# Kernel optimization log

Hardware: AMD Instinct MI355X
Metric: run time of the kernel (lower is better)

The kernel has to match this reference:

```python
import jax, jax.numpy as jnp
import numpy as np

N = 160000          # active voxels / points
C = 128             # embed_channels
K = 27              # 3x3x3 submanifold conv kernel volume
NUM_CLUSTERS = 2048
BN_EPS = 1e-5


def setup_inputs() -> dict:
    key = jax.random.key(0)
    ks = jax.random.split(key, 16)
    s = 0.05
    inp = {
        "feat": jax.random.normal(ks[0], (N, C), jnp.float32),
        "cluster0": jax.random.randint(ks[1], (N,), 0, NUM_CLUSTERS, jnp.int32),
        "cluster1": jax.random.randint(ks[2], (N,), 0, NUM_CLUSTERS, jnp.int32),
        "cluster2": jax.random.randint(ks[3], (N,), 0, NUM_CLUSTERS, jnp.int32),
        "nbr_idx": jax.random.randint(ks[4], (N, K), 0, N, jnp.int32),
        "nbr_mask": jax.random.randint(ks[5], (N, K), 0, 2, jnp.int32) > 0,
        "lw_W": jax.random.normal(ks[6], (3, C, C), jnp.float32) * s,
        "lw_gamma": jnp.ones((3, C), jnp.float32),
        "lw_beta": jnp.zeros((3, C), jnp.float32),
        "w_W": jax.random.normal(ks[7], (3, C, C), jnp.float32) * s,
        "proj_W": jax.random.normal(ks[8], (4, C, C), jnp.float32) * s,
        "proj_gamma": jnp.ones((4, C), jnp.float32),
        "proj_beta": jnp.zeros((4, C), jnp.float32),
        "adaptive_W": jax.random.normal(ks[9], (C, 3), jnp.float32) * s,
        "fuse_W": jax.random.normal(ks[10], (2 * C, C), jnp.float32) * s,
        "fuse_gamma": jnp.ones((C,), jnp.float32),
        "fuse_beta": jnp.zeros((C,), jnp.float32),
        "conv_W": jax.random.normal(ks[11], (2, K, C, C), jnp.float32) * 0.02,
        "conv_gamma": jnp.ones((2, C), jnp.float32),
        "conv_beta": jnp.zeros((2, C), jnp.float32),
    }
    return inp


def _bn(x, gamma, beta):
    # BatchNorm1d, training mode: per-channel stats over points, biased var
    m = jnp.mean(x, axis=0)
    v = jnp.var(x, axis=0)
    return (x - m) * jax.lax.rsqrt(v + BN_EPS) * gamma + beta


def _seg_sum(x, seg):
    return jax.ops.segment_sum(x, seg, num_segments=NUM_CLUSTERS)


def _seg_mean(x, seg):
    s = _seg_sum(x, seg)
    cnt = jax.ops.segment_sum(jnp.ones((x.shape[0], 1), x.dtype), seg,
                              num_segments=NUM_CLUSTERS)
    return s / jnp.maximum(cnt, 1.0)


def _subm_conv(x, W, nbr_idx, nbr_mask):
    # submanifold 3x3x3 conv on active sites: masked gather + per-offset GEMM
    m = nbr_mask.astype(x.dtype)  # [N, K]
    out = jnp.zeros_like(x)
    for k in range(K):
        out = out + (x[nbr_idx[:, k]] * m[:, k:k + 1]) @ W[k]
    return out


def reference(feat, cluster0, cluster1, cluster2, nbr_idx, nbr_mask,
              lw_W, lw_gamma, lw_beta, w_W, proj_W, proj_gamma, proj_beta,
              adaptive_W, fuse_W, fuse_gamma, fuse_beta,
              conv_W, conv_gamma, conv_beta):
    clusters = [cluster0, cluster1, cluster2]
    feats = []
    for i, cl in enumerate(clusters):
        pw = jax.nn.relu(_bn(feat @ lw_W[i], lw_gamma[i], lw_beta[i]))
        pw = pw - _seg_mean(pw, cl)[cl]
        pw = pw @ w_W[i]
        pw = jnp.exp(pw - jnp.max(pw))                      # global max
        pw = pw / (_seg_sum(pw, cl)[cl] + 1e-6)
        pfeat = jax.nn.relu(_bn(feat @ proj_W[i], proj_gamma[i], proj_beta[i])) * pw
        pfeat = _seg_sum(pfeat, cl)[cl]
        feats.append(pfeat)

    adp = jax.nn.softmax(feat @ adaptive_W, axis=1)          # [N, 3]
    feats = jnp.stack(feats, axis=1)                         # [N, 3, C]
    fused_branch = jnp.einsum('ln,lnc->lc', adp, feats)

    f = jax.nn.relu(_bn(feat @ proj_W[3], proj_gamma[3], proj_beta[3]))
    f = jnp.concatenate([f, fused_branch], axis=1)           # [N, 2C]
    f = jax.nn.relu(_bn(f @ fuse_W, fuse_gamma, fuse_beta)) + feat

    res = f
    h = _subm_conv(f, conv_W[0], nbr_idx, nbr_mask)
    h = jax.nn.relu(_bn(h, conv_gamma[0], conv_beta[0]))
    h = _subm_conv(h, conv_W[1], nbr_idx, nbr_mask)
    h = _bn(h, conv_gamma[1], conv_beta[1])
    return jax.nn.relu(h + res)
```

## Files before the change

kernel.cpp:

```cpp
#include <hip/hip_runtime.h>
#include <stdint.h>

#define N_PTS 160000
#define C 128
#define K27 27
#define NCLU 2048
#define BN_EPS 1e-5f
#define KP 136
#define KP2 264

typedef float f32x4 __attribute__((ext_vector_type(4)));
typedef short s16x8 __attribute__((ext_vector_type(8)));

__device__ __forceinline__ float bf2f(unsigned short u){
  union { unsigned int i; float f; } v; v.i = ((unsigned int)u) << 16; return v.f;
}
__device__ __forceinline__ unsigned short f2bf(float f){
  union { float f; unsigned int i; } v; v.f = f;
  unsigned int u = v.i;
  u += 0x7FFFu + ((u >> 16) & 1u);
  return (unsigned short)(u >> 16);
}
__device__ __forceinline__ unsigned int pk(float a, float b){
  return (unsigned int)f2bf(a) | ((unsigned int)f2bf(b) << 16);
}
__device__ __forceinline__ void up2(int w, float& a, float& b){
  a = bf2f((unsigned short)(w & 0xFFFF));
  b = bf2f((unsigned short)(((unsigned int)w) >> 16));
}
__device__ __forceinline__ unsigned int encf(float f){
  union { float f; unsigned int i; } v; v.f = f;
  return ((int)v.i < 0) ? ~v.i : (v.i | 0x80000000u);
}
__device__ __forceinline__ float decf(unsigned int e){
  union { unsigned int i; float f; } v;
  v.i = ((int)e < 0) ? (e ^ 0x80000000u) : ~e;
  return v.f;
}
__device__ __forceinline__ void bn_coef(const float* st, const float* gamma, const float* beta,
                                        int c, float& sc, float& sh){
  float mean = st[c] * (1.0f / N_PTS);
  float var  = st[C + c] * (1.0f / N_PTS) - mean * mean;
  float g = gamma[c] * rsqrtf(fmaxf(var, 0.f) + BN_EPS);
  sc = g; sh = beta[c] - mean * g;
}

__global__ void k_prep_weights(const float* __restrict__ lw, const float* __restrict__ w,
                               const float* __restrict__ proj, const float* __restrict__ conv,
                               const float* __restrict__ fuse,
                               unsigned short* __restrict__ tlw, unsigned short* __restrict__ tw,
                               unsigned short* __restrict__ tproj, unsigned short* __restrict__ tconv,
                               unsigned short* __restrict__ tfuse)
{
  int z = blockIdx.x, tid = threadIdx.x;
  if (z < 64){
    const float* src; unsigned short* dst; bool swz = false;
    if (z < 3){ src = lw + z*16384; dst = tlw + z*16384; }
    else if (z < 6){ src = w + (z-3)*16384; dst = tw + (z-3)*16384; }
    else if (z < 10){ src = proj + (z-6)*16384; dst = tproj + (z-6)*16384; }
    else { src = conv + (z-10)*16384; dst = tconv + (z-10)*16384; swz = true; }
    for (int i = tid; i < 16384; i += 256){
      int n = i >> 7, k = i & 127;
      int pos = swz ? (n*128 + (((k >> 3) ^ (n & 7)) << 3) + (k & 7)) : i;
      dst[pos] = f2bf(src[k*128 + n]);
    }
  } else {
    for (int i = tid; i < 32768; i += 256){
      int n = i >> 8, k = i & 255;
      tfuse[i] = f2bf(fuse[k*128 + n]);
    }
  }
}

__global__ void k_detect_mask(const unsigned int* __restrict__ mw, int* __restrict__ mmode)
{
  __shared__ int flag;
  if (threadIdx.x == 0) flag = 0;
  __syncthreads();
  for (int i = threadIdx.x; i < 4096; i += 256)
    if (mw[i] > 1u) flag = 1;
  __syncthreads();
  if (threadIdx.x == 0) *mmode = flag;
}

__global__ void k_hist(const int* __restrict__ c0, const int* __restrict__ c1,
                       const int* __restrict__ c2, int* __restrict__ hist)
{
  int idx = blockIdx.x*blockDim.x + threadIdx.x;
  int stride = gridDim.x*blockDim.x;
  for (; idx < 3*N_PTS; idx += stride){
    int j = idx / N_PTS, r = idx - j*N_PTS;
    const int* cp = (j==0)?c0:((j==1)?c1:c2);
    atomicAdd(&hist[j*NCLU + cp[r]], 1);
  }
}

__global__ void k_prefix(const int* __restrict__ hist, int* __restrict__ starts,
                         int* __restrict__ cursor)
{
  int j = blockIdx.x, tid = threadIdx.x;
  __shared__ int buf[NCLU];
  __shared__ int csum[256];
  for (int i = tid; i < NCLU; i += 256) buf[i] = hist[j*NCLU + i];
  __syncthreads();
  int s = 0;
  #pragma unroll
  for (int k = 0; k < 8; k++) s += buf[tid*8 + k];
  csum[tid] = s;
  __syncthreads();
  if (tid == 0){
    int run = 0;
    for (int i = 0; i < 256; i++){ int t = csum[i]; csum[i] = run; run += t; }
  }
  __syncthreads();
  int acc = csum[tid];
  #pragma unroll
  for (int k = 0; k < 8; k++){
    int i = tid*8 + k;
    starts[j*(NCLU+1) + i] = acc;
    cursor[j*NCLU + i] = acc;
    acc += buf[i];
  }
  if (tid == 255) starts[j*(NCLU+1) + NCLU] = acc;
}

__global__ void k_scatter(const int* __restrict__ c0, const int* __restrict__ c1,
                          const int* __restrict__ c2, int* __restrict__ cursor,
                          int* __restrict__ perm)
{
  int idx = blockIdx.x*blockDim.x + threadIdx.x;
  int stride = gridDim.x*blockDim.x;
  for (; idx < 3*N_PTS; idx += stride){
    int j = idx / N_PTS, r = idx - j*N_PTS;
    const int* cp = (j==0)?c0:((j==1)?c1:c2);
    int cl = cp[r];
    int slot = atomicAdd(&cursor[j*NCLU + cl], 1);
    perm[j*N_PTS + slot] = r;
  }
}

template<int V>
__global__ void k_seg(const unsigned short* __restrict__ X, const unsigned short* __restrict__ X2,
                      const int* __restrict__ perm, const int* __restrict__ starts,
                      const float* __restrict__ st, const float* __restrict__ gamma,
                      const float* __restrict__ beta, const unsigned int* __restrict__ genc,
                      const float* __restrict__ S2, float* __restrict__ S)
{
  __shared__ float red[16*128];
  const int cl = blockIdx.x;
  const int p0 = starts[cl], p1 = starts[cl+1];
  const int g = threadIdx.x >> 4, s = threadIdx.x & 15;
  const int c0 = s * 8;
  float sc[8], sh[8], den[8];
  if (V == 0 || V == 2){
    #pragma unroll
    for (int j = 0; j < 8; j++) bn_coef(st, gamma, beta, c0 + j, sc[j], sh[j]);
  }
  float gm = 0.f;
  if (V >= 1) gm = decf(*genc);
  if (V == 2){
    #pragma unroll
    for (int j = 0; j < 8; j++) den[j] = S2[cl*C + c0 + j] + 1e-6f;
  }
  float acc[8];
  #pragma unroll
  for (int j = 0; j < 8; j++) acc[j] = 0.f;
  for (int p = p0 + g; p < p1; p += 16){
    int row = perm[p];
    int4 v = *(const int4*)(X + (size_t)row*C + c0);
    float f[8];
    up2(v.x, f[0], f[1]); up2(v.y, f[2], f[3]); up2(v.z, f[4], f[5]); up2(v.w, f[6], f[7]);
    if (V == 0){
      #pragma unroll
      for (int j = 0; j < 8; j++) acc[j] += fmaxf(f[j]*sc[j] + sh[j], 0.f);
    } else if (V == 1){
      #pragma unroll
      for (int j = 0; j < 8; j++) acc[j] += __expf(f[j] - gm);
    } else {
      int4 v2 = *(const int4*)(X2 + (size_t)row*C + c0);
      float x2[8];
      up2(v2.x, x2[0], x2[1]); up2(v2.y, x2[2], x2[3]); up2(v2.z, x2[4], x2[5]); up2(v2.w, x2[6], x2[7]);
      #pragma unroll
      for (int j = 0; j < 8; j++)
        acc[j] += fmaxf(f[j]*sc[j] + sh[j], 0.f) * __expf(x2[j] - gm) / den[j];
    }
  }
  #pragma unroll
  for (int j = 0; j < 8; j++) red[g*128 + c0 + j] = acc[j];
  __syncthreads();
  if (threadIdx.x < 128){
    float t = 0.f;
    #pragma unroll
    for (int gg = 0; gg < 16; gg++) t += red[gg*128 + threadIdx.x];
    S[cl*C + threadIdx.x] = t;
  }
}

__global__ void k_adp(const float* __restrict__ feat, const float* __restrict__ aW,
                      float* __restrict__ adp, unsigned short* __restrict__ featb)
{
  __shared__ float wsh[384];
  int tid = threadIdx.x;
  for (int i = tid; i < 384; i += 256) wsh[i] = aW[i];
  __syncthreads();
  int gidx = blockIdx.x*256 + tid;
  int stride = gridDim.x*256;
  for (int t4 = gidx; t4 < N_PTS*4; t4 += stride){
    int row = t4 >> 2, part = t4 & 3;
    float e0=0.f, e1=0.f, e2=0.f;
    const float* fr = feat + (size_t)row*C + part*32;
    unsigned int pb[16];
    #pragma unroll
    for (int c = 0; c < 32; c += 4){
      float4 v = *(const float4*)(fr + c);
      int cc = part*32 + c;
      e0 += v.x*wsh[cc*3+0] + v.y*wsh[(cc+1)*3+0] + v.z*wsh[(cc+2)*3+0] + v.w*wsh[(cc+3)*3+0];
      e1 += v.x*wsh[cc*3+1] + v.y*wsh[(cc+1)*3+1] + v.z*wsh[(cc+2)*3+1] + v.w*wsh[(cc+3)*3+1];
      e2 += v.x*wsh[cc*3+2] + v.y*wsh[(cc+1)*3+2] + v.z*wsh[(cc+2)*3+2] + v.w*wsh[(cc+3)*3+2];
      pb[(c>>1)]   = pk(v.x, v.y);
      pb[(c>>1)+1] = pk(v.z, v.w);
    }
    if (featb){
      int4* dst = (int4*)(featb + (size_t)row*C + part*32);
      dst[0] = make_int4(pb[0], pb[1], pb[2], pb[3]);
      dst[1] = make_int4(pb[4], pb[5], pb[6], pb[7]);
      dst[2] = make_int4(pb[8], pb[9], pb[10], pb[11]);
      dst[3] = make_int4(pb[12], pb[13], pb[14], pb[15]);
    }
    e0 += __shfl_xor(e0, 1); e0 += __shfl_xor(e0, 2);
    e1 += __shfl_xor(e1, 1); e1 += __shfl_xor(e1, 2);
    e2 += __shfl_xor(e2, 1); e2 += __shfl_xor(e2, 2);
    if (part == 0){
      float m = fmaxf(e0, fmaxf(e1, e2));
      float p0 = __expf(e0-m), p1 = __expf(e1-m), p2 = __expf(e2-m);
      float inv = 1.f/(p0+p1+p2);
      adp[row*3+0] = p0*inv; adp[row*3+1] = p1*inv; adp[row*3+2] = p2*inv;
    }
  }
}

__device__ __forceinline__ void gemm_stats_epi(float* csum, float* csq, float* sred,
                                               int wave, int l4, int l16, int tid,
                                               float* __restrict__ stats)
{
  #pragma unroll
  for (int t = 0; t < 8; t++){
    csum[t] += __shfl_xor(csum[t], 16); csum[t] += __shfl_xor(csum[t], 32);
    csq[t]  += __shfl_xor(csq[t], 16);  csq[t]  += __shfl_xor(csq[t], 32);
  }
  if (l4 == 0){
    #pragma unroll
    for (int t = 0; t < 8; t++){
      sred[wave*128 + t*16 + l16] = csum[t];
      sred[512 + wave*128 + t*16 + l16] = csq[t];
    }
  }
  __syncthreads();
  if (tid < 128){
    float s = 0.f, q = 0.f;
    #pragma unroll
    for (int w2 = 0; w2 < 4; w2++){ s += sred[w2*128 + tid]; q += sred[512 + w2*128 + tid]; }
    atomicAdd(&stats[tid], s);
    atomicAdd(&stats[C + tid], q);
  }
}

template<typename AT>
__device__ __forceinline__ void stage_A(const AT* __restrict__ A, unsigned short* As,
                                        int row0, int r, int s)
{
  #pragma unroll
  for (int p = 0; p < 4; p++){
    int rr = r + p * 16;
    if constexpr (sizeof(AT) == 2){
      *(int4*)(As + rr * KP + s * 8) =
        *(const int4*)((const unsigned short*)A + (size_t)(row0 + rr) * C + s * 8);
    } else {
      const float4* ap = (const float4*)((const float*)A + (size_t)(row0 + rr) * C + s * 8);
      float4 x = ap[0], y = ap[1];
      *(int4*)(As + rr * KP + s * 8) =
        make_int4(pk(x.x,x.y), pk(x.z,x.w), pk(y.x,y.y), pk(y.z,y.w));
    }
  }
}

template<typename AT>
__global__ __launch_bounds__(256, 3)
void k_gemm_plain(const AT* __restrict__ A, const unsigned short* __restrict__ Bt,
                  unsigned short* __restrict__ Out, float* __restrict__ stats)
{
  __shared__ unsigned short As[64 * KP];
  __shared__ unsigned short Bs[128 * KP];
  const int tid = threadIdx.x;
  const int row0 = blockIdx.x * 64;
  const int r = tid >> 4, s = tid & 15;
  stage_A<AT>(A, As, row0, r, s);
  #pragma unroll
  for (int p = 0; p < 8; p++){
    int nn = r + p * 16;
    *(int4*)(Bs + nn * KP + s * 8) = *(const int4*)(Bt + nn * C + s * 8);
  }
  __syncthreads();
  const int lane = tid & 63, wave = tid >> 6;
  const int l16 = lane & 15, l4 = lane >> 4, m0 = wave * 16;
  f32x4 acc[8];
  #pragma unroll
  for (int t = 0; t < 8; t++) acc[t] = (f32x4){0.f,0.f,0.f,0.f};
  #pragma unroll
  for (int kk = 0; kk < 4; kk++){
    s16x8 a = *(const s16x8*)(As + (m0 + l16) * KP + kk * 32 + l4 * 8);
    #pragma unroll
    for (int t = 0; t < 8; t++){
      s16x8 b = *(const s16x8*)(Bs + (t * 16 + l16) * KP + kk * 32 + l4 * 8);
      acc[t] = __builtin_amdgcn_mfma_f32_16x16x32_bf16(a, b, acc[t], 0, 0, 0);
    }
  }
  float csum[8], csq[8];
  #pragma unroll
  for (int t = 0; t < 8; t++){
    float ss = 0.f, qq = 0.f;
    #pragma unroll
    for (int q = 0; q < 4; q++){
      float v = acc[t][q];
      int grow = row0 + m0 + l4 * 4 + q;
      Out[(size_t)grow * C + t * 16 + l16] = f2bf(v);
      ss += v; qq += v*v;
    }
    csum[t] = ss; csq[t] = qq;
  }
  __syncthreads();
  gemm_stats_epi(csum, csq, (float*)As, wave, l4, l16, tid, stats);
}

template<typename AT>
__global__ __launch_bounds__(256, 3)
void k_gemm_dual(const AT* __restrict__ A,
                 const unsigned short* __restrict__ Bt0, const unsigned short* __restrict__ Bt1,
                 unsigned short* __restrict__ Out0, unsigned short* __restrict__ Out1,
                 float* __restrict__ stats0, float* __restrict__ stats1)
{
  __shared__ unsigned short As[64 * KP];
  __shared__ unsigned short Bs[128 * KP];
  const int tid = threadIdx.x;
  const int row0 = blockIdx.x * 64;
  const int r = tid >> 4, s = tid & 15;
  const int lane = tid & 63, wave = tid >> 6;
  const int l16 = lane & 15, l4 = lane >> 4, m0 = wave * 16;

  stage_A<AT>(A, As, row0, r, s);
  #pragma unroll
  for (int p = 0; p < 8; p++){
    int nn = r + p * 16;
    *(int4*)(Bs + nn * KP + s * 8) = *(const int4*)(Bt0 + nn * C + s * 8);
  }
  __syncthreads();

  f32x4 acc[8];
  float csum0[8], csq0[8], csum1[8], csq1[8];

  #pragma unroll
  for (int t = 0; t < 8; t++) acc[t] = (f32x4){0.f,0.f,0.f,0.f};
  #pragma unroll
  for (int kk = 0; kk < 4; kk++){
    s16x8 a = *(const s16x8*)(As + (m0 + l16) * KP + kk * 32 + l4 * 8);
    #pragma unroll
    for (int t = 0; t < 8; t++){
      s16x8 b = *(const s16x8*)(Bs + (t * 16 + l16) * KP + kk * 32 + l4 * 8);
      acc[t] = __builtin_amdgcn_mfma_f32_16x16x32_bf16(a, b, acc[t], 0, 0, 0);
    }
  }
  #pragma unroll
  for (int t = 0; t < 8; t++){
    float ss = 0.f, qq = 0.f;
    #pragma unroll
    for (int q = 0; q < 4; q++){
      float v = acc[t][q];
      int grow = row0 + m0 + l4 * 4 + q;
      Out0[(size_t)grow * C + t * 16 + l16] = f2bf(v);
      ss += v; qq += v*v;
    }
    csum0[t] = ss; csq0[t] = qq;
  }
  __syncthreads();
  #pragma unroll
  for (int p = 0; p < 8; p++){
    int nn = r + p * 16;
    *(int4*)(Bs + nn * KP + s * 8) = *(const int4*)(Bt1 + nn * C + s * 8);
  }
  __syncthreads();

  #pragma unroll
  for (int t = 0; t < 8; t++) acc[t] = (f32x4){0.f,0.f,0.f,0.f};
  #pragma unroll
  for (int kk = 0; kk < 4; kk++){
    s16x8 a = *(const s16x8*)(As + (m0 + l16) * KP + kk * 32 + l4 * 8);
    #pragma unroll
    for (int t = 0; t < 8; t++){
      s16x8 b = *(const s16x8*)(Bs + (t * 16 + l16) * KP + kk * 32 + l4 * 8);
      acc[t] = __builtin_amdgcn_mfma_f32_16x16x32_bf16(a, b, acc[t], 0, 0, 0);
    }
  }
  #pragma unroll
  for (int t = 0; t < 8; t++){
    float ss = 0.f, qq = 0.f;
    #pragma unroll
    for (int q = 0; q < 4; q++){
      float v = acc[t][q];
      int grow = row0 + m0 + l4 * 4 + q;
      Out1[(size_t)grow * C + t * 16 + l16] = f2bf(v);
      ss += v; qq += v*v;
    }
    csum1[t] = ss; csq1[t] = qq;
  }
  __syncthreads();
  gemm_stats_epi(csum0, csq0, (float*)As, wave, l4, l16, tid, stats0);
  __syncthreads();
  gemm_stats_epi(csum1, csq1, (float*)As, wave, l4, l16, tid, stats1);
}

__global__ __launch_bounds__(256, 3)
void k_gemm_center(const unsigned short* __restrict__ PW, const unsigned short* __restrict__ Bt,
                   const int* __restrict__ cla, const float* __restrict__ S1,
                   const int* __restrict__ cnt, const float* __restrict__ st,
                   const float* __restrict__ gamma, const float* __restrict__ beta,
                   unsigned short* __restrict__ Out, unsigned int* __restrict__ gmax)
{
  __shared__ unsigned short As[64 * KP];
  __shared__ unsigned short Bs[128 * KP];
  __shared__ float wred[4];
  const int tid = threadIdx.x;
  const int row0 = blockIdx.x * 64;
  const int r = tid >> 4, s = tid & 15;
  float sc[8], sh[8];
  #pragma unroll
  for (int j = 0; j < 8; j++) bn_coef(st, gamma, beta, s*8 + j, sc[j], sh[j]);
  #pragma unroll
  for (int p = 0; p < 4; p++){
    int rr = r + p * 16;
    int grow = row0 + rr;
    int cl = cla[grow];
    float inv = 1.f / fmaxf(1.f, (float)cnt[cl]);
    int4 v = *(const int4*)(PW + (size_t)grow * C + s * 8);
    const float4* mp = (const float4*)(S1 + cl * C + s * 8);
    float4 ma = mp[0], mb = mp[1];
    float f[8];
    up2(v.x, f[0], f[1]); up2(v.y, f[2], f[3]); up2(v.z, f[4], f[5]); up2(v.w, f[6], f[7]);
    float m8[8] = {ma.x,ma.y,ma.z,ma.w,mb.x,mb.y,mb.z,mb.w};
    float o[8];
    #pragma unroll
    for (int j = 0; j < 8; j++) o[j] = fmaxf(f[j]*sc[j] + sh[j], 0.f) - m8[j]*inv;
    *(int4*)(As + rr * KP + s * 8) = make_int4(pk(o[0],o[1]), pk(o[2],o[3]), pk(o[4],o[5]), pk(o[6],o[7]));
  }
  #pragma unroll
  for (int p = 0; p < 8; p++){
    int nn = r + p * 16;
    *(int4*)(Bs + nn * KP + s * 8) = *(const int4*)(Bt + nn * C + s * 8);
  }
  __syncthreads();
  const int lane = tid & 63, wave = tid >> 6;
  const int l16 = lane & 15, l4 = lane >> 4, m0 = wave * 16;
  f32x4 acc[8];
  #pragma unroll
  for (int t = 0; t < 8; t++) acc[t] = (f32x4){0.f,0.f,0.f,0.f};
  #pragma unroll
  for (int kk = 0; kk < 4; kk++){
    s16x8 a = *(const s16x8*)(As + (m0 + l16) * KP + kk * 32 + l4 * 8);
    #pragma unroll
    for (int t = 0; t < 8; t++){
      s16x8 b = *(const s16x8*)(Bs + (t * 16 + l16) * KP + kk * 32 + l4 * 8);
      acc[t] = __builtin_amdgcn_mfma_f32_16x16x32_bf16(a, b, acc[t], 0, 0, 0);
    }
  }
  float mx = -3.4e38f;
  #pragma unroll
  for (int t = 0; t < 8; t++){
    #pragma unroll
    for (int q = 0; q < 4; q++){
      int grow = row0 + m0 + l4 * 4 + q;
      unsigned short ob = f2bf(acc[t][q]);
      Out[(size_t)grow * C + t * 16 + l16] = ob;
      mx = fmaxf(mx, bf2f(ob));
    }
  }
  #pragma unroll
  for (int off = 32; off; off >>= 1) mx = fmaxf(mx, __shfl_xor(mx, off));
  if ((tid & 63) == 0) wred[tid >> 6] = mx;
  __syncthreads();
  if (tid == 0){
    float m = fmaxf(fmaxf(wred[0], wred[1]), fmaxf(wred[2], wred[3]));
    atomicMax(gmax, encf(m));
  }
}

__global__ __launch_bounds__(256, 2)
void k_gemm_fuse(const unsigned short* __restrict__ XP3, const float* __restrict__ adp,
                 const int* __restrict__ cl0, const int* __restrict__ cl1,
                 const int* __restrict__ cl2, const float* __restrict__ S3,
                 const float* __restrict__ st, const float* __restrict__ gamma,
                 const float* __restrict__ beta, const unsigned short* __restrict__ Bt,
                 unsigned short* __restrict__ Out, float* __restrict__ stats)
{
  __shared__ unsigned short As[64 * KP2];
  __shared__ unsigned short Bs[128 * KP];
  __shared__ float scs[C], shs[C];
  const int tid = threadIdx.x;
  if (tid < C){ float a, b; bn_coef(st, gamma, beta, tid, a, b); scs[tid] = a; shs[tid] = b; }
  __syncthreads();
  const int row0 = blockIdx.x * 64;
  const int r8 = tid >> 5, s = tid & 31;
  const int r = tid >> 4, s16i = tid & 15;
  #pragma unroll
  for (int p = 0; p < 8; p++){
    int rr = r8 + p * 8;
    int grow = row0 + rr;
    if (s < 16){
      int c0 = s * 8;
      int4 v = *(const int4*)(XP3 + (size_t)grow * C + c0);
      float f0,f1,f2,f3,f4,f5,f6,f7;
      up2(v.x,f0,f1); up2(v.y,f2,f3); up2(v.z,f4,f5); up2(v.w,f6,f7);
      float o0 = fmaxf(f0*scs[c0+0]+shs[c0+0],0.f), o1 = fmaxf(f1*scs[c0+1]+shs[c0+1],0.f);
      float o2 = fmaxf(f2*scs[c0+2]+shs[c0+2],0.f), o3 = fmaxf(f3*scs[c0+3]+shs[c0+3],0.f);
      float o4 = fmaxf(f4*scs[c0+4]+shs[c0+4],0.f), o5 = fmaxf(f5*scs[c0+5]+shs[c0+5],0.f);
      float o6 = fmaxf(f6*scs[c0+6]+shs[c0+6],0.f), o7 = fmaxf(f7*scs[c0+7]+shs[c0+7],0.f);
      *(int4*)(As + rr * KP2 + c0) = make_int4(pk(o0,o1), pk(o2,o3), pk(o4,o5), pk(o6,o7));
    } else {
      int c0 = (s - 16) * 8;
      float a0 = adp[grow*3+0], a1 = adp[grow*3+1], a2 = adp[grow*3+2];
      const float* p0 = S3 + (size_t)cl0[grow] * C + c0;
      const float* p1 = S3 + (size_t)NCLU * C + (size_t)cl1[grow] * C + c0;
      const float* p2 = S3 + (size_t)2 * NCLU * C + (size_t)cl2[grow] * C + c0;
      float o[8];
      #pragma unroll
      for (int j = 0; j < 8; j++) o[j] = a0*p0[j] + a1*p1[j] + a2*p2[j];
      *(int4*)(As + rr * KP2 + 128 + c0) = make_int4(pk(o[0],o[1]), pk(o[2],o[3]), pk(o[4],o[5]), pk(o[6],o[7]));
    }
  }
  const int lane = tid & 63, wave = tid >> 6;
  const int l16 = lane & 15, l4 = lane >> 4, m0 = wave * 16;
  f32x4 acc[8];
  #pragma unroll
  for (int t = 0; t < 8; t++) acc[t] = (f32x4){0.f,0.f,0.f,0.f};
  #pragma unroll
  for (int h = 0; h < 2; h++){
    if (h) __syncthreads();
    #pragma unroll
    for (int p = 0; p < 8; p++){
      int nn = r + p * 16;
      *(int4*)(Bs + nn * KP + s16i * 8) = *(const int4*)(Bt + nn * 256 + h * 128 + s16i * 8);
    }
    __syncthreads();
    #pragma unroll
    for (int kk = 0; kk < 4; kk++){
      s16x8 a = *(const s16x8*)(As + (m0 + l16) * KP2 + h * 128 + kk * 32 + l4 * 8);
      #pragma unroll
      for (int t = 0; t < 8; t++){
        s16x8 b = *(const s16x8*)(Bs + (t * 16 + l16) * KP + kk * 32 + l4 * 8);
        acc[t] = __builtin_amdgcn_mfma_f32_16x16x32_bf16(a, b, acc[t], 0, 0, 0);
      }
    }
  }
  float csum[8], csq[8];
  #pragma unroll
  for (int t = 0; t < 8; t++){
    float ss = 0.f, qq = 0.f;
    #pragma unroll
    for (int q = 0; q < 4; q++){
      float v = acc[t][q];
      int grow = row0 + m0 + l4 * 4 + q;
      Out[(size_t)grow * C + t * 16 + l16] = f2bf(v);
      ss += v; qq += v*v;
    }
    csum[t] = ss; csq[t] = qq;
  }
  __syncthreads();
  gemm_stats_epi(csum, csq, (float*)As, wave, l4, l16, tid, stats);
}

__device__ __forceinline__ int ld_midx(const int* __restrict__ nbr, const void* __restrict__ maskp,
                                       int mm, int g){
  bool on = mm ? (((const unsigned char*)maskp)[g] != 0)
               : (((const int*)maskp)[g] != 0);
  int v = nbr[g];
  return on ? v : -1;
}

template<typename OT>
__global__ __launch_bounds__(512, 2)
void k_conv(const unsigned short* __restrict__ In, const unsigned short* __restrict__ Wt,
            const int* __restrict__ nbr, const void* __restrict__ maskp,
            const int* __restrict__ mmode, OT* __restrict__ Out, float* __restrict__ stats)
{
  __shared__ unsigned short Bs[2][128*128];
  const int tid = threadIdx.x;
  const int lane = tid & 63, wave = tid >> 6;
  const int l16 = lane & 15, l4 = lane >> 4;
  const int row0 = blockIdx.x * 256;
  const int mm = *mmode;
  const int r0g = row0 + wave*32 + l16;
  const int r1g = r0g + 16;
  const s16x8 z8 = (s16x8){0,0,0,0,0,0,0,0};

  auto stage_B = [&](int buf, int k){
    const char* gsrc = (const char*)(Wt + k*16384);
    char* lbase = (char*)&Bs[buf][0];
    #pragma unroll
    for (int p = 0; p < 4; p++){
      int chunk = p*512 + wave*64;
      __builtin_amdgcn_global_load_lds(
        (const unsigned int*)(gsrc + (size_t)(chunk + lane)*16),
        (unsigned int*)(lbase + (size_t)chunk*16), 16, 0, 0);
    }
  };

  f32x4 acc0[8], acc1[8];
  #pragma unroll
  for (int t = 0; t < 8; t++){ acc0[t] = (f32x4){0.f,0.f,0.f,0.f}; acc1[t] = (f32x4){0.f,0.f,0.f,0.f}; }

  s16x8 A0[8], A1[8];
  auto gather = [&](s16x8* dA, int gi0, int gi1){
    #pragma unroll
    for (int kk = 0; kk < 4; kk++){
      dA[kk]   = (gi0 >= 0) ? *(const s16x8*)(In + (size_t)gi0*C + kk*32 + l4*8) : z8;
      dA[kk+4] = (gi1 >= 0) ? *(const s16x8*)(In + (size_t)gi1*C + kk*32 + l4*8) : z8;
    }
  };
  auto compute = [&](const s16x8* a, int buf){
    #pragma unroll
    for (int kk = 0; kk < 4; kk++){
      #pragma unroll
      for (int t = 0; t < 8; t++){
        int n = t*16 + l16;
        s16x8 b = *(const s16x8*)(&Bs[buf][n*128 + ((((kk<<2)|l4) ^ (n & 7)) << 3)]);
        acc0[t] = __builtin_amdgcn_mfma_f32_16x16x32_bf16(a[kk],   b, acc0[t], 0, 0, 0);
        acc1[t] = __builtin_amdgcn_mfma_f32_16x16x32_bf16(a[kk+4], b, acc1[t], 0, 0, 0);
      }
    }
  };

  stage_B(0, 0);
  int i0 = ld_midx(nbr, maskp, mm, r0g*K27 + 0);
  int i1 = ld_midx(nbr, maskp, mm, r1g*K27 + 0);
  gather(A0, i0, i1);
  i0 = ld_midx(nbr, maskp, mm, r0g*K27 + 1);
  i1 = ld_midx(nbr, maskp, mm, r1g*K27 + 1);
  __syncthreads();

  #pragma unroll 1
  for (int kb = 0; kb < 13; kb++){
    const int k = kb * 2;
    stage_B(1, k + 1);
    gather(A1, i0, i1);
    i0 = ld_midx(nbr, maskp, mm, r0g*K27 + k + 2);
    i1 = ld_midx(nbr, maskp, mm, r1g*K27 + k + 2);
    compute(A0, 0);
    __syncthreads();
    stage_B(0, k + 2);
    gather(A0, i0, i1);
    if (kb < 12){
      i0 = ld_midx(nbr, maskp, mm, r0g*K27 + k + 3);
      i1 = ld_midx(nbr, maskp, mm, r1g*K27 + k + 3);
    }
    compute(A1, 1);
    __syncthreads();
  }
  compute(A0, 0);

  float csum[8], csq[8];
  #pragma unroll
  for (int t = 0; t < 8; t++){
    float ss = 0.f, qq = 0.f;
    #pragma unroll
    for (int q = 0; q < 4; q++){
      float v = acc0[t][q];
      int grow = row0 + wave*32 + l4*4 + q;
      if constexpr (sizeof(OT) == 2) Out[(size_t)grow * C + t*16 + l16] = f2bf(v);
      else                           Out[(size_t)grow * C + t*16 + l16] = v;
      ss += v; qq += v*v;
    }
    #pragma unroll
    for (int q = 0; q < 4; q++){
      float v = acc1[t][q];
      int grow = row0 + wave*32 + 16 + l4*4 + q;
      if constexpr (sizeof(OT) == 2) Out[(size_t)grow * C + t*16 + l16] = f2bf(v);
      else                           Out[(size_t)grow * C + t*16 + l16] = v;
      ss += v; qq += v*v;
    }
    csum[t] = ss; csq[t] = qq;
  }
  #pragma unroll
  for (int t = 0; t < 8; t++){
    csum[t] += __shfl_xor(csum[t], 16); csum[t] += __shfl_xor(csum[t], 32);
    csq[t]  += __shfl_xor(csq[t], 16);  csq[t]  += __shfl_xor(csq[t], 32);
  }
  __syncthreads();
  float* sred = (float*)Bs;
  if (l4 == 0){
    #pragma unroll
    for (int t = 0; t < 8; t++){
      sred[wave*128 + t*16 + l16] = csum[t];
      sred[1024 + wave*128 + t*16 + l16] = csq[t];
    }
  }
  __syncthreads();
  if (tid < 128){
    float s = 0.f, q = 0.f;
    #pragma unroll
    for (int w2 = 0; w2 < 8; w2++){ s += sred[w2*128 + tid]; q += sred[1024 + w2*128 + tid]; }
    atomicAdd(&stats[tid], s);
    atomicAdd(&stats[C + tid], q);
  }
}

template<int RELU>
__global__ void k_bnapply(const unsigned short* __restrict__ X, unsigned short* __restrict__ Y,
                          const float* __restrict__ st, const float* __restrict__ gamma,
                          const float* __restrict__ beta)
{
  const int total = N_PTS * 16;
  for (int idx = blockIdx.x*blockDim.x + threadIdx.x; idx < total; idx += gridDim.x*blockDim.x){
    int c0 = (idx & 15) * 8;
    int4 v = *(const int4*)(X + (size_t)idx * 8);
    float f[8];
    up2(v.x, f[0], f[1]); up2(v.y, f[2], f[3]); up2(v.z, f[4], f[5]); up2(v.w, f[6], f[7]);
    float o[8];
    #pragma unroll
    for (int j = 0; j < 8; j++){
      float sc, sh; bn_coef(st, gamma, beta, c0 + j, sc, sh);
      float t = f[j] * sc + sh;
      if (RELU) t = fmaxf(t, 0.f);
      o[j] = t;
    }
    *(int4*)(Y + (size_t)idx * 8) = make_int4(pk(o[0],o[1]), pk(o[2],o[3]), pk(o[4],o[5]), pk(o[6],o[7]));
  }
}

__global__ void k_fres(const unsigned short* __restrict__ G, const float* __restrict__ st,
                       const float* __restrict__ gamma, const float* __restrict__ beta,
                       const float* __restrict__ feat, unsigned short* __restrict__ FB)
{
  const int total = N_PTS * 16;
  for (int idx = blockIdx.x*blockDim.x + threadIdx.x; idx < total; idx += gridDim.x*blockDim.x){
    int c0 = (idx & 15) * 8;
    int4 v = *(const int4*)(G + (size_t)idx * 8);
    float f[8];
    up2(v.x, f[0], f[1]); up2(v.y, f[2], f[3]); up2(v.z, f[4], f[5]); up2(v.w, f[6], f[7]);
    const float4* fp = (const float4*)(feat + (size_t)idx * 8);
    float4 fa = fp[0], fb4 = fp[1];
    float fe[8] = {fa.x,fa.y,fa.z,fa.w,fb4.x,fb4.y,fb4.z,fb4.w};
    float o[8];
    #pragma unroll
    for (int j = 0; j < 8; j++){
      float sc, sh; bn_coef(st, gamma, beta, c0 + j, sc, sh);
      o[j] = fmaxf(f[j]*sc + sh, 0.f) + fe[j];
    }
    *(int4*)(FB + (size_t)idx * 8) = make_int4(pk(o[0],o[1]), pk(o[2],o[3]), pk(o[4],o[5]), pk(o[6],o[7]));
  }
}

__global__ void k_final(float* __restrict__ H2, const float* __restrict__ st,
                        const float* __restrict__ gamma, const float* __restrict__ beta,
                        const unsigned short* __restrict__ FB)
{
  const int total = N_PTS * 16;
  for (int idx = blockIdx.x*blockDim.x + threadIdx.x; idx < total; idx += gridDim.x*blockDim.x){
    int c0 = (idx & 15) * 8;
    float4* hp = (float4*)(H2 + (size_t)idx * 8);
    float4 a = hp[0], b = hp[1];
    int4 vf = *(const int4*)(FB + (size_t)idx * 8);
    float fr[8];
    up2(vf.x, fr[0], fr[1]); up2(vf.y, fr[2], fr[3]); up2(vf.z, fr[4], fr[5]); up2(vf.w, fr[6], fr[7]);
    float h[8] = {a.x,a.y,a.z,a.w,b.x,b.y,b.z,b.w};
    #pragma unroll
    for (int j = 0; j < 8; j++){
      float sc, sh; bn_coef(st, gamma, beta, c0 + j, sc, sh);
      h[j] = fmaxf(h[j]*sc + sh + fr[j], 0.f);
    }
    hp[0] = make_float4(h[0],h[1],h[2],h[3]);
    hp[1] = make_float4(h[4],h[5],h[6],h[7]);
  }
}

extern "C" void kernel_launch(void* const* d_in, const int* in_sizes, int n_in,
                              void* d_out, int out_size, void* d_ws, size_t ws_size,
                              hipStream_t stream)
{
  (void)in_sizes; (void)n_in; (void)out_size;
  const float* feat   = (const float*)d_in[0];
  const int* cls[3]   = {(const int*)d_in[1], (const int*)d_in[2], (const int*)d_in[3]};
  const int* nbr      = (const int*)d_in[4];
  const void* mask    = d_in[5];
  const float* lw_W   = (const float*)d_in[6];
  const float* lw_g   = (const float*)d_in[7];
  const float* lw_b   = (const float*)d_in[8];
  const float* w_W    = (const float*)d_in[9];
  const float* proj_W = (const float*)d_in[10];
  const float* proj_g = (const float*)d_in[11];
  const float* proj_b = (const float*)d_in[12];
  const float* adW    = (const float*)d_in[13];
  const float* fuse_W = (const float*)d_in[14];
  const float* fuse_g = (const float*)d_in[15];
  const float* fuse_b = (const float*)d_in[16];
  const float* conv_W = (const float*)d_in[17];
  const float* conv_g = (const float*)d_in[18];
  const float* conv_b = (const float*)d_in[19];

  char* w = (char*)d_ws;
  float*          stats  = (float*)(w + 0);
  unsigned int*   gmax   = (unsigned int*)(w + 10240);
  int*            mmode  = (int*)(w + 10240 + 16);
  int*            hist   = (int*)(w + 10496);
  int*            starts = (int*)(w + 35072);
  int*            cursor = (int*)(w + 59904);
  int*            perm   = (int*)(w + 84480);
  float*          S1     = (float*)(w + 2004480);
  float*          S2     = (float*)(w + 3053056);
  float*          S3     = (float*)(w + 4101632);
  float*          adp    = (float*)(w + 7247360);
  unsigned short* tlw    = (unsigned short*)(w + 9167360);
  unsigned short* tw     = (unsigned short*)(w + 9265664);
  unsigned short* tproj  = (unsigned short*)(w + 9363968);
  unsigned short* tfuse  = (unsigned short*)(w + 9495040);
  unsigned short* tconv  = (unsigned short*)(w + 9560576);
  unsigned short* B1     = (unsigned short*)(w + 11330048);
  unsigned short* B2     = (unsigned short*)(w + 52290048);
  unsigned short* B3     = (unsigned short*)(w + 93250048);
  const bool useb = ws_size >= (size_t)175170048;
  unsigned short* featb = useb ? (unsigned short*)(w + 134210048) : nullptr;

  hipMemsetAsync(d_ws, 0, 35072, stream);

  k_prep_weights<<<65, 256, 0, stream>>>(lw_W, w_W, proj_W, conv_W, fuse_W,
                                         tlw, tw, tproj, tconv, tfuse);
  k_detect_mask<<<1, 256, 0, stream>>>((const unsigned int*)mask, mmode);
  k_hist<<<1024, 256, 0, stream>>>(cls[0], cls[1], cls[2], hist);
  k_prefix<<<3, 256, 0, stream>>>(hist, starts, cursor);
  k_scatter<<<1024, 256, 0, stream>>>(cls[0], cls[1], cls[2], cursor, perm);
  k_adp<<<2500, 256, 0, stream>>>(feat, adW, adp, featb);

  if (useb) k_gemm_plain<unsigned short><<<2500, 256, 0, stream>>>(featb, tlw, B1, stats);
  else      k_gemm_plain<float><<<2500, 256, 0, stream>>>(feat, tlw, B1, stats);

  for (int i = 0; i < 3; i++){
    k_seg<0><<<2048, 256, 0, stream>>>(B1, nullptr, perm + i*N_PTS, starts + i*(NCLU+1),
                                       stats + i*256, lw_g + i*C, lw_b + i*C, nullptr, nullptr, S1);
    k_gemm_center<<<2500, 256, 0, stream>>>(B1, tw + i*16384, cls[i], S1, hist + i*NCLU,
                                            stats + i*256, lw_g + i*C, lw_b + i*C, B3, gmax + i);
    k_seg<1><<<2048, 256, 0, stream>>>(B3, nullptr, perm + i*N_PTS, starts + i*(NCLU+1),
                                       nullptr, nullptr, nullptr, gmax + i, nullptr, S2);
    const unsigned short* w0 = tproj + i*16384;
    const unsigned short* w1 = (i < 2) ? (tlw + (i+1)*16384) : (tproj + 3*16384);
    float* st1 = (i < 2) ? (stats + (i+1)*256) : (stats + 6*256);
    if (useb) k_gemm_dual<unsigned short><<<2500, 256, 0, stream>>>(featb, w0, w1, B2, B1,
                                                                    stats + (3+i)*256, st1);
    else      k_gemm_dual<float><<<2500, 256, 0, stream>>>(feat, w0, w1, B2, B1,
                                                           stats + (3+i)*256, st1);
    k_seg<2><<<2048, 256, 0, stream>>>(B2, B3, perm + i*N_PTS, starts + i*(NCLU+1),
                                       stats + (3+i)*256, proj_g + i*C, proj_b + i*C,
                                       gmax + i, S2, S3 + (size_t)i*NCLU*C);
  }

  k_gemm_fuse<<<2500, 256, 0, stream>>>(B1, adp, cls[0], cls[1], cls[2], S3,
                                        stats + 6*256, proj_g + 3*C, proj_b + 3*C, tfuse,
                                        B2, stats + 7*256);
  k_fres<<<2048, 256, 0, stream>>>(B2, stats + 7*256, fuse_g, fuse_b, feat, B3);

  k_conv<unsigned short><<<625, 512, 0, stream>>>(B3, tconv, nbr, mask, mmode, B1, stats + 8*256);
  k_bnapply<1><<<2048, 256, 0, stream>>>(B1, B2, stats + 8*256, conv_g, conv_b);
  k_conv<float><<<625, 512, 0, stream>>>(B2, tconv + 27*16384, nbr, mask, mmode,
                                         (float*)d_out, stats + 9*256);
  k_final<<<2048, 256, 0, stream>>>((float*)d_out, stats + 9*256, conv_g + C, conv_b + C, B3);
}
```

Baseline: 1.380 ms.

## Fuse softmax-denominator and weighted segment sums; halve conv rows per block

The separate exp-sum segment kernel is merged into a new per-cluster kernel. It first computes the softmax denominator in shared memory, then does the weighted pooled sum in a second pass over the same cluster rows. This removes one launch per branch and the S2 global round trip, at the cost of reading X2 twice within the block. Separately, the submanifold conv now handles 128 rows per block instead of 256, with one accumulator set and a launch-bounds hint of 4 blocks. This trades fewer registers and more blocks for twice as many weight stagings into LDS overall.

```diff
diff --git a/kernel.cpp b/kernel.cpp
--- a/kernel.cpp
+++ b/kernel.cpp
@@ -140,28 +140,19 @@
 }
 
 template<int V>
-__global__ void k_seg(const unsigned short* __restrict__ X, const unsigned short* __restrict__ X2,
+__global__ void k_seg(const unsigned short* __restrict__ X,
                       const int* __restrict__ perm, const int* __restrict__ starts,
                       const float* __restrict__ st, const float* __restrict__ gamma,
-                      const float* __restrict__ beta, const unsigned int* __restrict__ genc,
-                      const float* __restrict__ S2, float* __restrict__ S)
+                      const float* __restrict__ beta, float* __restrict__ S)
 {
   __shared__ float red[16*128];
   const int cl = blockIdx.x;
   const int p0 = starts[cl], p1 = starts[cl+1];
   const int g = threadIdx.x >> 4, s = threadIdx.x & 15;
   const int c0 = s * 8;
-  float sc[8], sh[8], den[8];
-  if (V == 0 || V == 2){
-    #pragma unroll
-    for (int j = 0; j < 8; j++) bn_coef(st, gamma, beta, c0 + j, sc[j], sh[j]);
-  }
-  float gm = 0.f;
-  if (V >= 1) gm = decf(*genc);
-  if (V == 2){
-    #pragma unroll
-    for (int j = 0; j < 8; j++) den[j] = S2[cl*C + c0 + j] + 1e-6f;
-  }
+  float sc[8], sh[8];
+  #pragma unroll
+  for (int j = 0; j < 8; j++) bn_coef(st, gamma, beta, c0 + j, sc[j], sh[j]);
   float acc[8];
   #pragma unroll
   for (int j = 0; j < 8; j++) acc[j] = 0.f;
@@ -170,20 +161,8 @@
     int4 v = *(const int4*)(X + (size_t)row*C + c0);
     float f[8];
     up2(v.x, f[0], f[1]); up2(v.y, f[2], f[3]); up2(v.z, f[4], f[5]); up2(v.w, f[6], f[7]);
-    if (V == 0){
-      #pragma unroll
-      for (int j = 0; j < 8; j++) acc[j] += fmaxf(f[j]*sc[j] + sh[j], 0.f);
-    } else if (V == 1){
-      #pragma unroll
-      for (int j = 0; j < 8; j++) acc[j] += __expf(f[j] - gm);
-    } else {
-      int4 v2 = *(const int4*)(X2 + (size_t)row*C + c0);
-      float x2[8];
-      up2(v2.x, x2[0], x2[1]); up2(v2.y, x2[2], x2[3]); up2(v2.z, x2[4], x2[5]); up2(v2.w, x2[6], x2[7]);
-      #pragma unroll
-      for (int j = 0; j < 8; j++)
-        acc[j] += fmaxf(f[j]*sc[j] + sh[j], 0.f) * __expf(x2[j] - gm) / den[j];
-    }
+    #pragma unroll
+    for (int j = 0; j < 8; j++) acc[j] += fmaxf(f[j]*sc[j] + sh[j], 0.f);
   }
   #pragma unroll
   for (int j = 0; j < 8; j++) red[g*128 + c0 + j] = acc[j];
@@ -193,6 +172,72 @@
     #pragma unroll
     for (int gg = 0; gg < 16; gg++) t += red[gg*128 + threadIdx.x];
     S[cl*C + threadIdx.x] = t;
+  }
+}
+
+__global__ void k_seg12(const unsigned short* __restrict__ XP, const unsigned short* __restrict__ X2,
+                        const int* __restrict__ perm, const int* __restrict__ starts,
+                        const float* __restrict__ st, const float* __restrict__ gamma,
+                        const float* __restrict__ beta, const unsigned int* __restrict__ genc,
+                        float* __restrict__ S3)
+{
+  __shared__ float red[16*128];
+  const int cl = blockIdx.x;
+  const int p0 = starts[cl], p1 = starts[cl+1];
+  const int g = threadIdx.x >> 4, s = threadIdx.x & 15;
+  const int c0 = s * 8;
+  const float gm = decf(*genc);
+  float sc[8], sh[8];
+  #pragma unroll
+  for (int j = 0; j < 8; j++) bn_coef(st, gamma, beta, c0 + j, sc[j], sh[j]);
+
+  float acc[8];
+  #pragma unroll
+  for (int j = 0; j < 8; j++) acc[j] = 0.f;
+  for (int p = p0 + g; p < p1; p += 16){
+    int row = perm[p];
+    int4 v2 = *(const int4*)(X2 + (size_t)row*C + c0);
+    float x2[8];
+    up2(v2.x, x2[0], x2[1]); up2(v2.y, x2[2], x2[3]); up2(v2.z, x2[4], x2[5]); up2(v2.w, x2[6], x2[7]);
+    #pragma unroll
+    for (int j = 0; j < 8; j++) acc[j] += __expf(x2[j] - gm);
+  }
+  #pragma unroll
+  for (int j = 0; j < 8; j++) red[g*128 + c0 + j] = acc[j];
+  __syncthreads();
+  if (threadIdx.x < 128){
+    float t = 0.f;
+    #pragma unroll
+    for (int gg = 0; gg < 16; gg++) t += red[gg*128 + threadIdx.x];
+    red[threadIdx.x] = t;
+  }
+  __syncthreads();
+  float den[8];
+  #pragma unroll
+  for (int j = 0; j < 8; j++) den[j] = red[c0 + j] + 1e-6f;
+  __syncthreads();
+
+  #pragma unroll
+  for (int j = 0; j < 8; j++) acc[j] = 0.f;
+  for (int p = p0 + g; p < p1; p += 16){
+    int row = perm[p];
+    int4 v  = *(const int4*)(XP + (size_t)row*C + c0);
+    int4 v2 = *(const int4*)(X2 + (size_t)row*C + c0);
+    float f[8], x2[8];
+    up2(v.x, f[0], f[1]); up2(v.y, f[2], f[3]); up2(v.z, f[4], f[5]); up2(v.w, f[6], f[7]);
+    up2(v2.x, x2[0], x2[1]); up2(v2.y, x2[2], x2[3]); up2(v2.z, x2[4], x2[5]); up2(v2.w, x2[6], x2[7]);
+    #pragma unroll
+    for (int j = 0; j < 8; j++)
+      acc[j] += fmaxf(f[j]*sc[j] + sh[j], 0.f) * __expf(x2[j] - gm) / den[j];
+  }
+  #pragma unroll
+  for (int j = 0; j < 8; j++) red[g*128 + c0 + j] = acc[j];
+  __syncthreads();
+  if (threadIdx.x < 128){
+    float t = 0.f;
+    #pragma unroll
+    for (int gg = 0; gg < 16; gg++) t += red[gg*128 + threadIdx.x];
+    S3[cl*C + threadIdx.x] = t;
   }
 }
 
@@ -585,7 +630,7 @@
 }
 
 template<typename OT>
-__global__ __launch_bounds__(512, 2)
+__global__ __launch_bounds__(512, 4)
 void k_conv(const unsigned short* __restrict__ In, const unsigned short* __restrict__ Wt,
             const int* __restrict__ nbr, const void* __restrict__ maskp,
             const int* __restrict__ mmode, OT* __restrict__ Out, float* __restrict__ stats)
@@ -594,10 +639,9 @@
   const int tid = threadIdx.x;
   const int lane = tid & 63, wave = tid >> 6;
   const int l16 = lane & 15, l4 = lane >> 4;
-  const int row0 = blockIdx.x * 256;
+  const int row0 = blockIdx.x * 128;
   const int mm = *mmode;
-  const int r0g = row0 + wave*32 + l16;
-  const int r1g = r0g + 16;
+  const int rg = row0 + wave*16 + l16;
   const s16x8 z8 = (s16x8){0,0,0,0,0,0,0,0};
 
   auto stage_B = [&](int buf, int k){
@@ -612,17 +656,15 @@
     }
   };
 
-  f32x4 acc0[8], acc1[8];
-  #pragma unroll
-  for (int t = 0; t < 8; t++){ acc0[t] = (f32x4){0.f,0.f,0.f,0.f}; acc1[t] = (f32x4){0.f,0.f,0.f,0.f}; }
-
-  s16x8 A0[8], A1[8];
-  auto gather = [&](s16x8* dA, int gi0, int gi1){
-    #pragma unroll
-    for (int kk = 0; kk < 4; kk++){
-      dA[kk]   = (gi0 >= 0) ? *(const s16x8*)(In + (size_t)gi0*C + kk*32 + l4*8) : z8;
-      dA[kk+4] = (gi1 >= 0) ? *(const s16x8*)(In + (size_t)gi1*C + kk*32 + l4*8) : z8;
-    }
+  f32x4 acc[8];
+  #pragma unroll
+  for (int t = 0; t < 8; t++) acc[t] = (f32x4){0.f,0.f,0.f,0.f};
+
+  s16x8 A0[4], A1[4];
+  auto gather = [&](s16x8* dA, int gi){
+    #pragma unroll
+    for (int kk = 0; kk < 4; kk++)
+      dA[kk] = (gi >= 0) ? *(const s16x8*)(In + (size_t)gi*C + kk*32 + l4*8) : z8;
   };
   auto compute = [&](const s16x8* a, int buf){
     #pragma unroll
@@ -631,35 +673,28 @@
       for (int t = 0; t < 8; t++){
         int n = t*16 + l16;
         s16x8 b = *(const s16x8*)(&Bs[buf][n*128 + ((((kk<<2)|l4) ^ (n & 7)) << 3)]);
-        acc0[t] = __builtin_amdgcn_mfma_f32_16x16x32_bf16(a[kk],   b, acc0[t], 0, 0, 0);
-        acc1[t] = __builtin_amdgcn_mfma_f32_16x16x32_bf16(a[kk+4], b, acc1[t], 0, 0, 0);
+        acc[t] = __builtin_amdgcn_mfma_f32_16x16x32_bf16(a[kk], b, acc[t], 0, 0, 0);
       }
     }
   };
 
   stage_B(0, 0);
-  int i0 = ld_midx(nbr, maskp, mm, r0g*K27 + 0);
-  int i1 = ld_midx(nbr, maskp, mm, r1g*K27 + 0);
-  gather(A0, i0, i1);
-  i0 = ld_midx(nbr, maskp, mm, r0g*K27 + 1);
-  i1 = ld_midx(nbr, maskp, mm, r1g*K27 + 1);
+  int i0 = ld_midx(nbr, maskp, mm, rg*K27 + 0);
+  gather(A0, i0);
+  i0 = ld_midx(nbr, maskp, mm, rg*K27 + 1);
   __syncthreads();
 
   #pragma unroll 1
   for (int kb = 0; kb < 13; kb++){
     const int k = kb * 2;
     stage_B(1, k + 1);
-    gather(A1, i0, i1);
-    i0 = ld_midx(nbr, maskp, mm, r0g*K27 + k + 2);
-    i1 = ld_midx(nbr, maskp, mm, r1g*K27 + k + 2);
+    gather(A1, i0);
+    i0 = ld_midx(nbr, maskp, mm, rg*K27 + k + 2);
     compute(A0, 0);
     __syncthreads();
     stage_B(0, k + 2);
-    gather(A0, i0, i1);
-    if (kb < 12){
-      i0 = ld_midx(nbr, maskp, mm, r0g*K27 + k + 3);
-      i1 = ld_midx(nbr, maskp, mm, r1g*K27 + k + 3);
-    }
+    gather(A0, i0);
+    if (kb < 12) i0 = ld_midx(nbr, maskp, mm, rg*K27 + k + 3);
     compute(A1, 1);
     __syncthreads();
   }
@@ -671,16 +706,8 @@
     float ss = 0.f, qq = 0.f;
     #pragma unroll
     for (int q = 0; q < 4; q++){
-      float v = acc0[t][q];
-      int grow = row0 + wave*32 + l4*4 + q;
-      if constexpr (sizeof(OT) == 2) Out[(size_t)grow * C + t*16 + l16] = f2bf(v);
-      else                           Out[(size_t)grow * C + t*16 + l16] = v;
-      ss += v; qq += v*v;
-    }
-    #pragma unroll
-    for (int q = 0; q < 4; q++){
-      float v = acc1[t][q];
-      int grow = row0 + wave*32 + 16 + l4*4 + q;
+      float v = acc[t][q];
+      int grow = row0 + wave*16 + l4*4 + q;
       if constexpr (sizeof(OT) == 2) Out[(size_t)grow * C + t*16 + l16] = f2bf(v);
       else                           Out[(size_t)grow * C + t*16 + l16] = v;
       ss += v; qq += v*v;
@@ -813,7 +840,6 @@
   int*            cursor = (int*)(w + 59904);
   int*            perm   = (int*)(w + 84480);
   float*          S1     = (float*)(w + 2004480);
-  float*          S2     = (float*)(w + 3053056);
   float*          S3     = (float*)(w + 4101632);
   float*          adp    = (float*)(w + 7247360);
   unsigned short* tlw    = (unsigned short*)(w + 9167360);
@@ -841,12 +867,10 @@
   else      k_gemm_plain<float><<<2500, 256, 0, stream>>>(feat, tlw, B1, stats);
 
   for (int i = 0; i < 3; i++){
-    k_seg<0><<<2048, 256, 0, stream>>>(B1, nullptr, perm + i*N_PTS, starts + i*(NCLU+1),
-                                       stats + i*256, lw_g + i*C, lw_b + i*C, nullptr, nullptr, S1);
+    k_seg<0><<<2048, 256, 0, stream>>>(B1, perm + i*N_PTS, starts + i*(NCLU+1),
+                                       stats + i*256, lw_g + i*C, lw_b + i*C, S1);
     k_gemm_center<<<2500, 256, 0, stream>>>(B1, tw + i*16384, cls[i], S1, hist + i*NCLU,
                                             stats + i*256, lw_g + i*C, lw_b + i*C, B3, gmax + i);
-    k_seg<1><<<2048, 256, 0, stream>>>(B3, nullptr, perm + i*N_PTS, starts + i*(NCLU+1),
-                                       nullptr, nullptr, nullptr, gmax + i, nullptr, S2);
     const unsigned short* w0 = tproj + i*16384;
     const unsigned short* w1 = (i < 2) ? (tlw + (i+1)*16384) : (tproj + 3*16384);
     float* st1 = (i < 2) ? (stats + (i+1)*256) : (stats + 6*256);
@@ -854,9 +878,9 @@
                                                                     stats + (3+i)*256, st1);
     else      k_gemm_dual<float><<<2500, 256, 0, stream>>>(feat, w0, w1, B2, B1,
                                                            stats + (3+i)*256, st1);
-    k_seg<2><<<2048, 256, 0, stream>>>(B2, B3, perm + i*N_PTS, starts + i*(NCLU+1),
-                                       stats + (3+i)*256, proj_g + i*C, proj_b + i*C,
-                                       gmax + i, S2, S3 + (size_t)i*NCLU*C);
+    k_seg12<<<2048, 256, 0, stream>>>(B2, B3, perm + i*N_PTS, starts + i*(NCLU+1),
+                                      stats + (3+i)*256, proj_g + i*C, proj_b + i*C,
+                                      gmax + i, S3 + (size_t)i*NCLU*C);
   }
 
   k_gemm_fuse<<<2500, 256, 0, stream>>>(B1, adp, cls[0], cls[1], cls[2], S3,
@@ -864,9 +888,9 @@
                                         B2, stats + 7*256);
   k_fres<<<2048, 256, 0, stream>>>(B2, stats + 7*256, fuse_g, fuse_b, feat, B3);
 
-  k_conv<unsigned short><<<625, 512, 0, stream>>>(B3, tconv, nbr, mask, mmode, B1, stats + 8*256);
+  k_conv<unsigned short><<<1250, 512, 0, stream>>>(B3, tconv, nbr, mask, mmode, B1, stats + 8*256);
   k_bnapply<1><<<2048, 256, 0, stream>>>(B1, B2, stats + 8*256, conv_g, conv_b);
-  k_conv<float><<<625, 512, 0, stream>>>(B2, tconv + 27*16384, nbr, mask, mmode,
-                                         (float*)d_out, stats + 9*256);
+  k_conv<float><<<1250, 512, 0, stream>>>(B2, tconv + 27*16384, nbr, mask, mmode,
+                                          (float*)d_out, stats + 9*256);
   k_final<<<2048, 256, 0, stream>>>((float*)d_out, stats + 9*256, conv_g + C, conv_b + C, B3);
 }
```

Result: faster. 1.286 ms (-6.8%).
